# Performance work log

Hardware: AMD Instinct MI355X
Metric: run time of the kernel (lower is better)

The kernel has to match this reference:

```python
import jax, jax.numpy as jnp
import numpy as np

RESIDUAL_WEIGHT = 0.3
TEMPERATURE = 0.07
EPS = 1e-12


def setup_inputs() -> dict:
    key = jax.random.key(0)
    features = jax.random.normal(key, (4, 64, 64, 384), dtype=jnp.float32)
    return {"features": features}


def reference(features):
    B, H, W, D = features.shape
    x = features.reshape(B, H * W, D)                      # (B, N, D)
    # F.normalize(dim=-1): x / max(||x||, eps)
    norm = jnp.linalg.norm(x, axis=-1, keepdims=True)
    xn = x / jnp.maximum(norm, EPS)
    # cosine-similarity correlation matrix, scaled by temperature
    corr = jnp.einsum("bnd,bmd->bnm", xn, xn) / TEMPERATURE  # (B, N, N)
    attn = jax.nn.softmax(corr, axis=-1)
    attended = jnp.einsum("bnm,bmd->bnd", attn, x)         # (B, N, D)
    out = x + RESIDUAL_WEIGHT * attended
    return out.reshape(B, H, W, D)
```

## Files before the change

kernel.cpp:

```cpp
#include <hip/hip_runtime.h>
#include <hip/hip_bf16.h>
#include <stdint.h>

typedef __bf16 bf16_t;
typedef __bf16 bf16x8 __attribute__((ext_vector_type(8)));
typedef float f32x16 __attribute__((ext_vector_type(16)));

#define BB 4
#define NN 4096
#define DD 384
#define KBLK 64
#define NT (NN / KBLK)
#define NROWS (BB * NN)
#define SCALEC 20.609929155556627f

__global__ __launch_bounds__(256) void norm_kernel(const float* __restrict__ x,
                                                   bf16_t* __restrict__ xn) {
    int row  = blockIdx.x * 4 + (threadIdx.x >> 6);
    int lane = threadIdx.x & 63;
    const float* xr = x + (size_t)row * DD;
    float v[6];
    float ss = 0.f;
#pragma unroll
    for (int j = 0; j < 6; ++j) { v[j] = xr[lane + j * 64]; ss += v[j] * v[j]; }
#pragma unroll
    for (int m = 1; m < 64; m <<= 1) ss += __shfl_xor(ss, m);
    float inv = 1.0f / fmaxf(sqrtf(ss), 1e-12f);
    bf16_t* o = xn + (size_t)row * DD;
#pragma unroll
    for (int j = 0; j < 6; ++j) o[lane + j * 64] = (bf16_t)(v[j] * inv);
}

__global__ __launch_bounds__(256) void transpose_kernel(const float* __restrict__ x,
                                                        bf16_t* __restrict__ xvT) {
    int bid = blockIdx.x;
    int dt = bid % (DD / 64);
    int nt = (bid / (DD / 64)) % (NN / 64);
    int b  = bid / ((DD / 64) * (NN / 64));
    __shared__ float tile[64][65];
    int t = threadIdx.x;
    const float* src = x + ((size_t)b * NN + (size_t)nt * 64) * DD + dt * 64;
#pragma unroll
    for (int j = 0; j < 4; ++j) {
        int lin = j * 256 + t;
        int nl = lin >> 4;
        int dc = (lin & 15) * 4;
        const float4 f = *(const float4*)(src + (size_t)nl * DD + dc);
        tile[nl][dc + 0] = f.x; tile[nl][dc + 1] = f.y;
        tile[nl][dc + 2] = f.z; tile[nl][dc + 3] = f.w;
    }
    __syncthreads();
    bf16_t* dst = xvT + ((size_t)b * DD + (size_t)dt * 64) * NN + (size_t)nt * 64;
#pragma unroll
    for (int j = 0; j < 2; ++j) {
        int lin = j * 256 + t;
        int dl = lin >> 3;
        int nc = (lin & 7) * 8;
        bf16x8 v;
#pragma unroll
        for (int jj = 0; jj < 8; ++jj) v[jj] = (bf16_t)tile[nc + jj][dl];
        *(bf16x8*)(dst + (size_t)dl * NN + nc) = v;
    }
}

__device__ __forceinline__ void load_lds16(const void* g, void* l) {
    __builtin_amdgcn_global_load_lds((const __attribute__((address_space(1))) uint32_t*)g,
                                     (__attribute__((address_space(3))) uint32_t*)l,
                                     16, 0, 0);
}

template <bool SPLIT>
__global__ __launch_bounds__(256, 2) void attn_kernel(const float* __restrict__ x,
                                                      const bf16_t* __restrict__ xn,
                                                      const bf16_t* __restrict__ xvT,
                                                      float* __restrict__ out,
                                                      float* __restrict__ Opart,
                                                      float* __restrict__ lpart) {
    constexpr int TPS = SPLIT ? (NT / 2) : NT;
    __shared__ __align__(16) char Ks[49152];
    __shared__ __align__(16) char Pb[16384];

    const int tid = threadIdx.x;
    const int w = tid >> 6, l = tid & 63;
    const int l31 = l & 31, hi = l >> 5;
    const int qg = w >> 1, kh = w & 1;

    const int bid = blockIdx.x;
    int b, qi, s_idx;
    if (SPLIT) {
        b = (bid & 7) >> 1; s_idx = bid & 1; qi = bid >> 3;
    } else {
        b = (bid >> 1) & 3; s_idx = 0; qi = (bid >> 3) | ((bid & 1) << 5);
    }
    const int kt0 = s_idx * TPS;
    const int qrow0 = b * NN + qi * 64;

    const char* xnb  = (const char*)xn;
    const char* xvTb = (const char*)xvT;
    char* Ksb = (char*)Ks;
    char* Pbb = (char*)Pb;

    const bf16_t* qp = xn + (size_t)(qrow0 + qg * 32 + l31) * DD + hi * 8;
    bf16x8 qf[24];
#pragma unroll
    for (int c = 0; c < 24; ++c) qf[c] = *(const bf16x8*)(qp + c * 16);

    f32x16 O0, O1, O2, O3, O4, O5;
    O0 = 0.f; O1 = 0.f; O2 = 0.f; O3 = 0.f; O4 = 0.f; O5 = 0.f;
    float lacc = 0.f;

#define STAGE_K(KT) { \
    const size_t kg = ((size_t)b * NN + (size_t)(KT) * KBLK) * (DD * 2); \
    _Pragma("unroll") \
    for (int i = 0; i < 12; ++i) { \
        int idx = i * 256 + tid; int key = idx & 63; int c2h = idx >> 6; \
        load_lds16(xnb + kg + (size_t)key * (DD * 2) + c2h * 16, \
                   (void*)(Ksb + (size_t)(i * 256 + (w << 6)) * 16)); \
    } }

    STAGE_K(kt0);

    const char* kB = Ksb + (size_t)(hi * 64 + kh * 32 + l31) * 16;
    const int psw = (l31 & 15) << 4;
    const int rsrow = tid >> 2, rsseg = tid & 3;
    const int rswz = (rsrow & 15) << 4;
    const int kcol2 = (kh * 32 + l31) * 2;

#define VLD(DST, KC) { \
    _Pragma("unroll") \
    for (int dt = 0; dt < 3; ++dt) \
        DST[dt] = *(const bf16x8*)(vB + (size_t)dt * 32 * (NN * 2) + (KC) * 32); }

#define PV_STEP(VF, KC) { \
    bf16x8 pa0 = *(const bf16x8*)(Pbb + (l31) * 256 + (((KC) * 32 + hi * 16) ^ psw)); \
    bf16x8 pa1 = *(const bf16x8*)(Pbb + (32 + l31) * 256 + (((KC) * 32 + hi * 16) ^ psw)); \
    O0 = __builtin_amdgcn_mfma_f32_32x32x16_bf16(pa0, VF[0], O0, 0, 0, 0); \
    O1 = __builtin_amdgcn_mfma_f32_32x32x16_bf16(pa0, VF[1], O1, 0, 0, 0); \
    O2 = __builtin_amdgcn_mfma_f32_32x32x16_bf16(pa0, VF[2], O2, 0, 0, 0); \
    O3 = __builtin_amdgcn_mfma_f32_32x32x16_bf16(pa1, VF[0], O3, 0, 0, 0); \
    O4 = __builtin_amdgcn_mfma_f32_32x32x16_bf16(pa1, VF[1], O4, 0, 0, 0); \
    O5 = __builtin_amdgcn_mfma_f32_32x32x16_bf16(pa1, VF[2], O5, 0, 0, 0); }

    for (int t = 0; t < TPS; ++t) {
        const int kt = kt0 + t;
        const char* vB = xvTb + (((size_t)(b * DD + w * 96 + l31) * NN)
                                 + (size_t)kt * KBLK + hi * 8) * 2;
        asm volatile("s_waitcnt vmcnt(0)" ::: "memory");
        __builtin_amdgcn_sched_barrier(0);
        __builtin_amdgcn_s_barrier();
        __builtin_amdgcn_sched_barrier(0);

        f32x16 s = 0.f;
#pragma unroll
        for (int c = 0; c < 24; ++c) {
            bf16x8 kf = *(const bf16x8*)(kB + c * 2048);
            s = __builtin_amdgcn_mfma_f32_32x32x16_bf16(qf[c], kf, s, 0, 0, 0);
        }

        __builtin_amdgcn_sched_barrier(0);
        __builtin_amdgcn_s_barrier();
        __builtin_amdgcn_sched_barrier(0);

        {
            int ktn = kt + 1; if (ktn > NT - 1) ktn = NT - 1;
            STAGE_K(ktn);
        }
        __builtin_amdgcn_sched_barrier(0);

        bf16x8 vfA[3], vfB[3];
        VLD(vfA, 0);

#pragma unroll
        for (int r = 0; r < 16; ++r) {
            float p = exp2f(fmaf(s[r], SCALEC, -SCALEC));
            int q = qg * 32 + 4 * hi + (r & 3) + 8 * (r >> 2);
            int off = q * 256 + (kcol2 ^ ((q & 15) << 4));
            *(bf16_t*)(Pbb + off) = (bf16_t)p;
        }
        asm volatile("s_waitcnt lgkmcnt(0)" ::: "memory");
        __builtin_amdgcn_sched_barrier(0);
        __builtin_amdgcn_s_barrier();
        __builtin_amdgcn_sched_barrier(0);

        VLD(vfB, 1);
        {
            const char* rb = Pbb + rsrow * 256;
            bf16x8 a = *(const bf16x8*)(rb + ((rsseg * 32) ^ rswz));
            bf16x8 c = *(const bf16x8*)(rb + ((rsseg * 32 + 16) ^ rswz));
            float ps = 0.f;
#pragma unroll
            for (int e = 0; e < 8; ++e) ps += (float)a[e] + (float)c[e];
            lacc += ps;
        }

        PV_STEP(vfA, 0);
        VLD(vfA, 2);
        PV_STEP(vfB, 1);
        VLD(vfB, 3);
        PV_STEP(vfA, 2);
        PV_STEP(vfB, 3);
    }
#undef STAGE_K
#undef VLD
#undef PV_STEP

    lacc += __shfl_xor(lacc, 1);
    lacc += __shfl_xor(lacc, 2);

    if (SPLIT) {
        if ((tid & 3) == 0) lpart[(size_t)s_idx * NROWS + qrow0 + rsrow] = lacc;
        float* Ob = Opart + (size_t)s_idx * NROWS * DD;
        const f32x16* Os[6] = {&O0, &O1, &O2, &O3, &O4, &O5};
#pragma unroll
        for (int g2 = 0; g2 < 2; ++g2) {
#pragma unroll
            for (int dt = 0; dt < 3; ++dt) {
                const f32x16& Ot = *Os[g2 * 3 + dt];
                int dcol = w * 96 + dt * 32 + l31;
#pragma unroll
                for (int r = 0; r < 16; ++r) {
                    int q = g2 * 32 + 4 * hi + (r & 3) + 8 * (r >> 2);
                    Ob[(size_t)(qrow0 + q) * DD + dcol] = Ot[r];
                }
            }
        }
    } else {
        __builtin_amdgcn_s_barrier();
        float* lb = (float*)Pbb;
        if ((tid & 3) == 0) lb[rsrow] = lacc;
        asm volatile("s_waitcnt lgkmcnt(0)" ::: "memory");
        __builtin_amdgcn_s_barrier();
        const f32x16* Os[6] = {&O0, &O1, &O2, &O3, &O4, &O5};
#pragma unroll
        for (int g2 = 0; g2 < 2; ++g2) {
#pragma unroll
            for (int dt = 0; dt < 3; ++dt) {
                const f32x16& Ot = *Os[g2 * 3 + dt];
                int dcol = w * 96 + dt * 32 + l31;
#pragma unroll
                for (int r = 0; r < 16; ++r) {
                    int q = g2 * 32 + 4 * hi + (r & 3) + 8 * (r >> 2);
                    size_t idx = (size_t)(qrow0 + q) * DD + dcol;
                    out[idx] = x[idx] + Ot[r] * (0.3f / lb[q]);
                }
            }
        }
    }
}

__global__ __launch_bounds__(256) void merge_kernel(const float* __restrict__ x,
                                                    const float* __restrict__ Opart,
                                                    const float* __restrict__ lpart,
                                                    float* __restrict__ out) {
    int row  = blockIdx.x * 4 + (threadIdx.x >> 6);
    int lane = threadIdx.x & 63;
    float lsum = lpart[row] + lpart[NROWS + row];
    float inv = 0.3f / lsum;
    size_t base = (size_t)row * DD;
    const float* O0 = Opart + base;
    const float* O1 = Opart + (size_t)NROWS * DD + base;
#pragma unroll
    for (int j = 0; j < 6; ++j) {
        int d = lane + j * 64;
        out[base + d] = x[base + d] + (O0[d] + O1[d]) * inv;
    }
}

extern "C" void kernel_launch(void* const* d_in, const int* in_sizes, int n_in,
                              void* d_out, int out_size, void* d_ws, size_t ws_size,
                              hipStream_t stream) {
    const float* x = (const float*)d_in[0];
    float* out = (float*)d_out;
    char* ws = (char*)d_ws;

    const size_t xn_bytes = (size_t)BB * NN * DD * 2;
    bf16_t* xn  = (bf16_t*)ws;
    bf16_t* xvT = (bf16_t*)(ws + xn_bytes);
    float* Opart = (float*)(ws + 2 * xn_bytes);
    const size_t Opart_bytes = (size_t)2 * NROWS * DD * 4;
    float* lpart = (float*)(ws + 2 * xn_bytes + Opart_bytes);
    const size_t need2 = 2 * xn_bytes + Opart_bytes + (size_t)2 * NROWS * 4;

    norm_kernel<<<(BB * NN) / 4, 256, 0, stream>>>(x, xn);
    transpose_kernel<<<BB * (NN / 64) * (DD / 64), 256, 0, stream>>>(x, xvT);
    if (ws_size >= need2) {
        attn_kernel<true><<<512, 256, 0, stream>>>(x, xn, xvT, out, Opart, lpart);
        merge_kernel<<<NROWS / 4, 256, 0, stream>>>(x, Opart, lpart, out);
    } else {
        attn_kernel<false><<<256, 256, 0, stream>>>(x, xn, xvT, out, nullptr, nullptr);
    }
}
```

Before: 342.9 us.

## Switch QK^T to 16x16x32 MFMA with per-wave 16-row query tiles

Reworks the score computation so each wave owns 16 query rows against all 64 keys, using 16x16x32 bf16 MFMAs with four accumulators instead of one 32x32x16 accumulator over half the keys. The query fragment register footprint halves (12 instead of 24 bf16x8), which may ease register pressure at two blocks per CU, and P-tile writes are remapped to the new layout. It also swaps exp2f for the raw hardware exp2 builtin. The risk is that the K LDS read pattern and layout mapping change bank-conflict behaviour, and the 16x16 MFMA issue pattern differs in throughput.

```diff
diff --git a/kernel.cpp b/kernel.cpp
--- a/kernel.cpp
+++ b/kernel.cpp
@@ -4,6 +4,7 @@
 
 typedef __bf16 bf16_t;
 typedef __bf16 bf16x8 __attribute__((ext_vector_type(8)));
+typedef float f32x4 __attribute__((ext_vector_type(4)));
 typedef float f32x16 __attribute__((ext_vector_type(16)));
 
 #define BB 4
@@ -83,7 +84,7 @@
     const int tid = threadIdx.x;
     const int w = tid >> 6, l = tid & 63;
     const int l31 = l & 31, hi = l >> 5;
-    const int qg = w >> 1, kh = w & 1;
+    const int lo16 = l & 15, g4 = l >> 4;
 
     const int bid = blockIdx.x;
     int b, qi, s_idx;
@@ -100,10 +101,10 @@
     char* Ksb = (char*)Ks;
     char* Pbb = (char*)Pb;
 
-    const bf16_t* qp = xn + (size_t)(qrow0 + qg * 32 + l31) * DD + hi * 8;
-    bf16x8 qf[24];
-#pragma unroll
-    for (int c = 0; c < 24; ++c) qf[c] = *(const bf16x8*)(qp + c * 16);
+    const bf16_t* qp = xn + (size_t)(qrow0 + w * 16 + lo16) * DD + g4 * 8;
+    bf16x8 qf[12];
+#pragma unroll
+    for (int c = 0; c < 12; ++c) qf[c] = *(const bf16x8*)(qp + c * 32);
 
     f32x16 O0, O1, O2, O3, O4, O5;
     O0 = 0.f; O1 = 0.f; O2 = 0.f; O3 = 0.f; O4 = 0.f; O5 = 0.f;
@@ -120,11 +121,11 @@
 
     STAGE_K(kt0);
 
-    const char* kB = Ksb + (size_t)(hi * 64 + kh * 32 + l31) * 16;
+    const char* kB = Ksb + (size_t)g4 * 1024 + lo16 * 16;
     const int psw = (l31 & 15) << 4;
     const int rsrow = tid >> 2, rsseg = tid & 3;
     const int rswz = (rsrow & 15) << 4;
-    const int kcol2 = (kh * 32 + l31) * 2;
+    const int qrow16 = w * 16 + g4 * 4;
 
 #define VLD(DST, KC) { \
     _Pragma("unroll") \
@@ -141,6 +142,15 @@
     O4 = __builtin_amdgcn_mfma_f32_32x32x16_bf16(pa1, VF[1], O4, 0, 0, 0); \
     O5 = __builtin_amdgcn_mfma_f32_32x32x16_bf16(pa1, VF[2], O5, 0, 0, 0); }
 
+#define SM_STEP(SS, KB) { \
+    _Pragma("unroll") \
+    for (int r = 0; r < 4; ++r) { \
+        float p = __builtin_amdgcn_exp2f(fmaf(SS[r], SCALEC, -SCALEC)); \
+        int q = qrow16 + r; \
+        int off = q * 256 + ((((KB) * 16 + lo16) * 2) ^ ((q & 15) << 4)); \
+        *(bf16_t*)(Pbb + off) = (bf16_t)p; \
+    } }
+
     for (int t = 0; t < TPS; ++t) {
         const int kt = kt0 + t;
         const char* vB = xvTb + (((size_t)(b * DD + w * 96 + l31) * NN)
@@ -150,11 +160,15 @@
         __builtin_amdgcn_s_barrier();
         __builtin_amdgcn_sched_barrier(0);
 
-        f32x16 s = 0.f;
-#pragma unroll
-        for (int c = 0; c < 24; ++c) {
-            bf16x8 kf = *(const bf16x8*)(kB + c * 2048);
-            s = __builtin_amdgcn_mfma_f32_32x32x16_bf16(qf[c], kf, s, 0, 0, 0);
+        f32x4 s0, s1, s2, s3;
+        s0 = 0.f; s1 = 0.f; s2 = 0.f; s3 = 0.f;
+#pragma unroll
+        for (int c = 0; c < 12; ++c) {
+            const char* kc = kB + c * 4096;
+            s0 = __builtin_amdgcn_mfma_f32_16x16x32_bf16(qf[c], *(const bf16x8*)(kc),       s0, 0, 0, 0);
+            s1 = __builtin_amdgcn_mfma_f32_16x16x32_bf16(qf[c], *(const bf16x8*)(kc + 256), s1, 0, 0, 0);
+            s2 = __builtin_amdgcn_mfma_f32_16x16x32_bf16(qf[c], *(const bf16x8*)(kc + 512), s2, 0, 0, 0);
+            s3 = __builtin_amdgcn_mfma_f32_16x16x32_bf16(qf[c], *(const bf16x8*)(kc + 768), s3, 0, 0, 0);
         }
 
         __builtin_amdgcn_sched_barrier(0);
@@ -170,13 +184,7 @@
         bf16x8 vfA[3], vfB[3];
         VLD(vfA, 0);
 
-#pragma unroll
-        for (int r = 0; r < 16; ++r) {
-            float p = exp2f(fmaf(s[r], SCALEC, -SCALEC));
-            int q = qg * 32 + 4 * hi + (r & 3) + 8 * (r >> 2);
-            int off = q * 256 + (kcol2 ^ ((q & 15) << 4));
-            *(bf16_t*)(Pbb + off) = (bf16_t)p;
-        }
+        SM_STEP(s0, 0); SM_STEP(s1, 1); SM_STEP(s2, 2); SM_STEP(s3, 3);
         asm volatile("s_waitcnt lgkmcnt(0)" ::: "memory");
         __builtin_amdgcn_sched_barrier(0);
         __builtin_amdgcn_s_barrier();
@@ -203,6 +211,7 @@
 #undef STAGE_K
 #undef VLD
 #undef PV_STEP
+#undef SM_STEP
 
     lacc += __shfl_xor(lacc, 1);
     lacc += __shfl_xor(lacc, 2);
```

New measurement: 744.4 us. 2.17x slower.
